# Optimization experiments

Measured on AMD Instinct MI355X. Metric: run time of the kernel, lower is better.

Reference implementation:

```python
import jax, jax.numpy as jnp
import numpy as np

B, S, H = 4, 2048, 1024
NH = 16
HD = H // NH  # 64
EPS = 1e-12


def setup_inputs() -> dict:
    key = jax.random.key(0)
    ks = jax.random.split(key, 10)
    sc = 1.0 / np.sqrt(H)
    return {
        "hidden_states": jax.random.normal(ks[0], (B, S, H), jnp.float32),
        "attention_mask": jnp.ones((B, S), jnp.float32),
        "Wq": jax.random.normal(ks[1], (H, H), jnp.float32) * sc,
        "bq": jnp.zeros((H,), jnp.float32),
        "Wk": jax.random.normal(ks[2], (H, H), jnp.float32) * sc,
        "bk": jnp.zeros((H,), jnp.float32),
        "Wv": jax.random.normal(ks[3], (H, H), jnp.float32) * sc,
        "bv": jnp.zeros((H,), jnp.float32),
        "Wd": jax.random.normal(ks[4], (H, H), jnp.float32) * sc,
        "bd": jnp.zeros((H,), jnp.float32),
        "ln_g": jnp.ones((H,), jnp.float32),
        "ln_b": jnp.zeros((H,), jnp.float32),
    }


def reference(hidden_states, attention_mask, Wq, bq, Wk, bk, Wv, bv, Wd, bd, ln_g, ln_b):
    def heads(x):  # [B,S,H] -> [B,NH,S,HD]
        return x.reshape(B, S, NH, HD).transpose(0, 2, 1, 3)

    q = heads(hidden_states @ Wq.T + bq)
    k = heads(hidden_states @ Wk.T + bk)
    v = heads(hidden_states @ Wv.T + bv)

    scores = jnp.einsum('bhqd,bhkd->bhqk', q, k) / np.sqrt(HD).astype(np.float32)
    # 2D mask -> [B,1,1,S]; (1-m)*-10000 additive bias
    bias = (1.0 - attention_mask)[:, None, None, :] * -10000.0
    probs = jax.nn.softmax(scores + bias, axis=-1)  # dropout p=0 -> identity

    ctx = jnp.einsum('bhqk,bhkd->bhqd', probs, v)
    ctx = ctx.transpose(0, 2, 1, 3).reshape(B, S, H)

    out = ctx @ Wd.T + bd
    x = out + hidden_states
    mu = jnp.mean(x, axis=-1, keepdims=True)
    var = jnp.mean(jnp.square(x - mu), axis=-1, keepdims=True)
    return (x - mu) * jax.lax.rsqrt(var + EPS) * ln_g + ln_b
```

## Files before the change

### kernel.cpp

```cpp
#include <hip/hip_runtime.h>
#include <stdint.h>

#define B_ 4
#define S_ 2048
#define H_ 1024
#define NH_ 16
#define HD_ 64

typedef __bf16 bf16x8 __attribute__((ext_vector_type(8)));
typedef unsigned short u16x8 __attribute__((ext_vector_type(8)));
typedef float f32x4 __attribute__((ext_vector_type(4)));
typedef float f32x16 __attribute__((ext_vector_type(16)));

__device__ __forceinline__ unsigned short f2bf(float x) {
  union { float f; unsigned u; } c; c.f = x;
  unsigned r = (c.u + 0x7FFFu + ((c.u >> 16) & 1u)) >> 16;
  return (unsigned short)r;
}

__device__ __forceinline__ void gload16(const unsigned short* g, unsigned short* lds) {
  __builtin_amdgcn_global_load_lds((const __attribute__((address_space(1))) void*)g,
                                   (__attribute__((address_space(3))) void*)lds, 16, 0, 0);
}

__global__ __launch_bounds__(256) void cvt_kernel(const float* __restrict__ src,
                                                  unsigned short* __restrict__ dst, int n) {
  int i = (blockIdx.x * blockDim.x + threadIdx.x) * 4;
  if (i < n) {
    float4 v = *reinterpret_cast<const float4*>(src + i);
    ushort4 o;
    o.x = f2bf(v.x); o.y = f2bf(v.y); o.z = f2bf(v.z); o.w = f2bf(v.w);
    *reinterpret_cast<ushort4*>(dst + i) = o;
  }
}

template <bool BF16OUT>
__global__ __launch_bounds__(256) void gemm_bt(const unsigned short* __restrict__ A,
                                               const unsigned short* __restrict__ Bm,
                                               const float* __restrict__ bias,
                                               void* __restrict__ Cout,
                                               int M, int N, int K) {
  __shared__ unsigned short As[128 * 32];
  __shared__ unsigned short Bs[128 * 32];
  const int t = threadIdx.x;
  const int lane = t & 63;
  const int wv = t >> 6;
  const int wm = wv >> 1, wn = wv & 1;
  const int m0 = blockIdx.x * 128, n0 = blockIdx.y * 128;
  const int l15 = lane & 15, g8 = (lane >> 4) * 8;

  f32x4 acc[4][4];
#pragma unroll
  for (int i = 0; i < 4; ++i)
#pragma unroll
    for (int j = 0; j < 4; ++j) { f32x4 z = {0.f, 0.f, 0.f, 0.f}; acc[i][j] = z; }

  const int rowA = t >> 2;
  const int colA = (t & 3) * 8;
  const unsigned short* gA0 = A + (long)(m0 + rowA) * K + colA;
  const unsigned short* gA1 = A + (long)(m0 + 64 + rowA) * K + colA;
  const unsigned short* gB0 = Bm + (long)(n0 + rowA) * K + colA;
  const unsigned short* gB1 = Bm + (long)(n0 + 64 + rowA) * K + colA;
  unsigned short* ldsA0 = &As[wv * 512];
  unsigned short* ldsA1 = &As[2048 + wv * 512];
  unsigned short* ldsB0 = &Bs[wv * 512];
  unsigned short* ldsB1 = &Bs[2048 + wv * 512];

  for (int k0 = 0; k0 < K; k0 += 32) {
    __syncthreads();
    gload16(gA0 + k0, ldsA0);
    gload16(gA1 + k0, ldsA1);
    gload16(gB0 + k0, ldsB0);
    gload16(gB1 + k0, ldsB1);
    __syncthreads();

    bf16x8 af[4], bfr[4];
#pragma unroll
    for (int i = 0; i < 4; ++i)
      af[i] = *reinterpret_cast<const bf16x8*>(&As[(wm * 64 + i * 16 + l15) * 32 + g8]);
#pragma unroll
    for (int j = 0; j < 4; ++j)
      bfr[j] = *reinterpret_cast<const bf16x8*>(&Bs[(wn * 64 + j * 16 + l15) * 32 + g8]);
#pragma unroll
    for (int i = 0; i < 4; ++i)
#pragma unroll
      for (int j = 0; j < 4; ++j)
        acc[i][j] = __builtin_amdgcn_mfma_f32_16x16x32_bf16(af[i], bfr[j], acc[i][j], 0, 0, 0);
  }

  const int r0 = (lane >> 4) * 4;
#pragma unroll
  for (int i = 0; i < 4; ++i)
#pragma unroll
    for (int j = 0; j < 4; ++j) {
      int col = n0 + wn * 64 + j * 16 + l15;
      float bv = bias[col];
#pragma unroll
      for (int r = 0; r < 4; ++r) {
        int row = m0 + wm * 64 + i * 16 + r0 + r;
        float v = acc[i][j][r] + bv;
        if (BF16OUT)
          ((unsigned short*)Cout)[(long)row * N + col] = f2bf(v);
        else
          ((float*)Cout)[(long)row * N + col] = v;
      }
    }
}

__global__ __launch_bounds__(256) void attn_kernel(const unsigned short* __restrict__ Q,
                                                   const unsigned short* __restrict__ Kg,
                                                   const unsigned short* __restrict__ Vg,
                                                   const float* __restrict__ mask,
                                                   unsigned short* __restrict__ ctx) {
  __shared__ __align__(16) unsigned short Kt[2][64 * 72];
  __shared__ __align__(16) unsigned short VtT[2][64 * 72];
  __shared__ __align__(16) float biasL[2][64];
  __shared__ __align__(16) float alBuf[4][32];
  __shared__ int mflag[2];

  const int t = threadIdx.x, lane = t & 63;
  const int wv = t >> 6;
  const int h = blockIdx.y, b = blockIdx.z;
  const int q0w = blockIdx.x * 128 + wv * 32;
  const int l31 = lane & 31, h2 = lane >> 5;
  const long headoff = (long)h * HD_;
  const float L2E = 1.44269504088896f;
  const float SC = 0.125f * L2E;

  bf16x8 qf[4];
  {
    const unsigned short* Qrow = Q + ((long)(b * S_ + q0w + l31)) * H_ + headoff;
#pragma unroll
    for (int c = 0; c < 4; ++c) {
      bf16x8 raw = *reinterpret_cast<const bf16x8*>(Qrow + 16 * c + 8 * h2);
#pragma unroll
      for (int j = 0; j < 8; ++j) qf[c][j] = (__bf16)((float)raw[j] * SC);
    }
  }

  f32x16 o[2];
#pragma unroll
  for (int dt = 0; dt < 2; ++dt)
#pragma unroll
    for (int r = 0; r < 16; ++r) o[dt][r] = 0.f;
  float mrow = -1.0e30f, lsum = 0.f;

  const int rowd0 = l31, rowd1 = 32 + l31;
  const int grp0 = (rowd0 >> 3) & 7, grp1 = (rowd1 >> 3) & 7;

  const int krow = t >> 3, kcg = (t & 7) * 8;
  const int vrow = (t >> 3) * 2, dc = t & 7;
  const long gbase = (long)(b * S_) * H_ + headoff;
  u16x8 kr0, kr1, vr0, vr1;
  float mv = 1.0f;

  auto LOADT = [&](int kv0) {
    kr0 = *reinterpret_cast<const u16x8*>(Kg + gbase + (long)(kv0 + krow) * H_ + kcg);
    kr1 = *reinterpret_cast<const u16x8*>(Kg + gbase + (long)(kv0 + krow + 32) * H_ + kcg);
    vr0 = *reinterpret_cast<const u16x8*>(Vg + gbase + (long)(kv0 + vrow) * H_ + dc * 8);
    vr1 = *reinterpret_cast<const u16x8*>(Vg + gbase + (long)(kv0 + vrow + 1) * H_ + dc * 8);
    if (t < 64) mv = mask[b * S_ + kv0 + t];
  };
  auto WRITET = [&](int buf) {
    *reinterpret_cast<u16x8*>(&Kt[buf][krow * 72 + kcg]) = kr0;
    *reinterpret_cast<u16x8*>(&Kt[buf][(krow + 32) * 72 + kcg]) = kr1;
    const int pos = (vrow & 7) | (((vrow >> 3) ^ dc) << 3);
#pragma unroll
    for (int j = 0; j < 8; ++j) {
      ushort2 pr; pr.x = vr0[j]; pr.y = vr1[j];
      *reinterpret_cast<ushort2*>(&VtT[buf][(dc * 8 + j) * 72 + pos]) = pr;
    }
    if (t < 64) {
      biasL[buf][t] = (1.f - mv) * (-10000.f * L2E);
      unsigned long long bal = __ballot(mv != 1.0f);
      if (t == 0) mflag[buf] = (bal != 0ull);
    }
  };

  const int NT = S_ / 64;
  LOADT(0);
  WRITET(0);
  __syncthreads();

  for (int it = 0; it < NT; ++it) {
    const int cur = it & 1;
    const bool more = (it + 1 < NT);
    if (more) LOADT((it + 1) * 64);

    const unsigned short* KtA = &Kt[cur][l31 * 72 + 8 * h2];
    const int mf = mflag[cur];

#pragma unroll
    for (int kvt = 0; kvt < 2; ++kvt) {
      f32x16 sv;
#pragma unroll
      for (int r = 0; r < 16; ++r) sv[r] = 0.f;
      __builtin_amdgcn_s_setprio(1);
#pragma unroll
      for (int c = 0; c < 4; ++c) {
        bf16x8 af = *reinterpret_cast<const bf16x8*>(KtA + (kvt * 32) * 72 + 16 * c);
        sv = __builtin_amdgcn_mfma_f32_32x32x16_bf16(af, qf[c], sv, 0, 0, 0);
      }
      __builtin_amdgcn_s_setprio(0);
      if (mf) {
#pragma unroll
        for (int m = 0; m < 4; ++m) {
          f32x4 bb = *reinterpret_cast<const f32x4*>(&biasL[cur][kvt * 32 + 8 * m + 4 * h2]);
#pragma unroll
          for (int i = 0; i < 4; ++i) sv[4 * m + i] += bb[i];
        }
      }
      float a0 = fmaxf(sv[0], sv[1]), a1 = fmaxf(sv[2], sv[3]);
      float a2 = fmaxf(sv[4], sv[5]), a3 = fmaxf(sv[6], sv[7]);
      float a4 = fmaxf(sv[8], sv[9]), a5 = fmaxf(sv[10], sv[11]);
      float a6 = fmaxf(sv[12], sv[13]), a7 = fmaxf(sv[14], sv[15]);
      float b0 = fmaxf(a0, a1), b1 = fmaxf(a2, a3), b2 = fmaxf(a4, a5), b3 = fmaxf(a6, a7);
      float tm = fmaxf(fmaxf(b0, b1), fmaxf(b2, b3));
      tm = fmaxf(tm, __shfl_xor(tm, 32));
      if (!__all(tm <= mrow + 8.0f)) {
        float mn = fmaxf(mrow, tm);
        float al = exp2f(mrow - mn);
        mrow = mn;
        lsum *= al;
        if (lane < 32) alBuf[wv][lane] = al;
        __builtin_amdgcn_wave_barrier();
#pragma unroll
        for (int m = 0; m < 4; ++m) {
          f32x4 av = *reinterpret_cast<const f32x4*>(&alBuf[wv][8 * m + 4 * h2]);
#pragma unroll
          for (int i = 0; i < 4; ++i) {
            o[0][4 * m + i] *= av[i];
            o[1][4 * m + i] *= av[i];
          }
        }
      }
#pragma unroll
      for (int r = 0; r < 16; ++r) sv[r] = exp2f(sv[r] - mrow);
      {
        float s0 = sv[0] + sv[1], s1 = sv[2] + sv[3], s2 = sv[4] + sv[5], s3 = sv[6] + sv[7];
        float s4 = sv[8] + sv[9], s5 = sv[10] + sv[11], s6 = sv[12] + sv[13], s7 = sv[14] + sv[15];
        float u0 = s0 + s1, u1 = s2 + s3, u2 = s4 + s5, u3 = s6 + s7;
        float ts = (u0 + u1) + (u2 + u3);
        ts += __shfl_xor(ts, 32);
        lsum += ts;
      }

#pragma unroll
      for (int c2 = 0; c2 < 2; ++c2) {
        int kc = 2 * kvt + c2;
        unsigned p0, p1, p2, p3;
        {
          union { __bf16 e[2]; unsigned w; } u;
          u.e[0] = (__bf16)sv[8 * c2 + 0]; u.e[1] = (__bf16)sv[8 * c2 + 1]; p0 = u.w;
          u.e[0] = (__bf16)sv[8 * c2 + 2]; u.e[1] = (__bf16)sv[8 * c2 + 3]; p1 = u.w;
          u.e[0] = (__bf16)sv[8 * c2 + 4]; u.e[1] = (__bf16)sv[8 * c2 + 5]; p2 = u.w;
          u.e[0] = (__bf16)sv[8 * c2 + 6]; u.e[1] = (__bf16)sv[8 * c2 + 7]; p3 = u.w;
        }
        asm("v_permlane32_swap_b32 %0, %1" : "+v"(p0), "+v"(p2));
        asm("v_permlane32_swap_b32 %0, %1" : "+v"(p1), "+v"(p3));
        union { unsigned w[4]; bf16x8 v; } fa;
        fa.w[0] = p0; fa.w[1] = p1; fa.w[2] = p2; fa.w[3] = p3;

        bf16x8 vb0 = *reinterpret_cast<const bf16x8*>(
            &VtT[cur][rowd0 * 72 + 8 * ((2 * kc + h2) ^ grp0)]);
        bf16x8 vb1 = *reinterpret_cast<const bf16x8*>(
            &VtT[cur][rowd1 * 72 + 8 * ((2 * kc + h2) ^ grp1)]);
        __builtin_amdgcn_s_setprio(1);
        o[0] = __builtin_amdgcn_mfma_f32_32x32x16_bf16(fa.v, vb0, o[0], 0, 0, 0);
        o[1] = __builtin_amdgcn_mfma_f32_32x32x16_bf16(fa.v, vb1, o[1], 0, 0, 0);
        __builtin_amdgcn_s_setprio(0);
      }
    }

    if (more) {
      WRITET(cur ^ 1);
      __syncthreads();
    }
  }

  if (lane < 32) alBuf[wv][lane] = 1.0f / lsum;
  __builtin_amdgcn_wave_barrier();
  unsigned short* ctxbase = ctx + ((long)(b * S_ + q0w + 4 * h2)) * H_ + headoff + l31;
#pragma unroll
  for (int m = 0; m < 4; ++m) {
    f32x4 iv = *reinterpret_cast<const f32x4*>(&alBuf[wv][8 * m + 4 * h2]);
#pragma unroll
    for (int i = 0; i < 4; ++i) {
#pragma unroll
      for (int dt = 0; dt < 2; ++dt)
        ctxbase[(long)(8 * m + i) * H_ + dt * 32] = f2bf(o[dt][4 * m + i] * iv[i]);
    }
  }
}

__global__ __launch_bounds__(256) void ln_kernel(const float* __restrict__ proj,
                                                 const float* __restrict__ hs,
                                                 const float* __restrict__ gam,
                                                 const float* __restrict__ bet,
                                                 float* __restrict__ out) {
  const int row = blockIdx.x;
  const int t = threadIdx.x;
  const long base = (long)row * H_ + t * 4;
  float4 a = *reinterpret_cast<const float4*>(proj + base);
  float4 hv = *reinterpret_cast<const float4*>(hs + base);
  float x0 = a.x + hv.x, x1 = a.y + hv.y, x2 = a.z + hv.z, x3 = a.w + hv.w;
  float s1 = x0 + x1 + x2 + x3;
  float s2 = x0 * x0 + x1 * x1 + x2 * x2 + x3 * x3;
#pragma unroll
  for (int off = 1; off < 64; off <<= 1) {
    s1 += __shfl_xor(s1, off);
    s2 += __shfl_xor(s2, off);
  }
  __shared__ float a1[4], a2[4];
  if ((t & 63) == 0) { a1[t >> 6] = s1; a2[t >> 6] = s2; }
  __syncthreads();
  float ts1 = a1[0] + a1[1] + a1[2] + a1[3];
  float ts2 = a2[0] + a2[1] + a2[2] + a2[3];
  float mu = ts1 * (1.0f / H_);
  float var = ts2 * (1.0f / H_) - mu * mu;
  float inv = rsqrtf(var + 1e-12f);
  float4 gv = *reinterpret_cast<const float4*>(gam + t * 4);
  float4 bb = *reinterpret_cast<const float4*>(bet + t * 4);
  float4 ov;
  ov.x = (x0 - mu) * inv * gv.x + bb.x;
  ov.y = (x1 - mu) * inv * gv.y + bb.y;
  ov.z = (x2 - mu) * inv * gv.z + bb.z;
  ov.w = (x3 - mu) * inv * gv.w + bb.w;
  *reinterpret_cast<float4*>(out + base) = ov;
}

extern "C" void kernel_launch(void* const* d_in, const int* in_sizes, int n_in,
                              void* d_out, int out_size, void* d_ws, size_t ws_size,
                              hipStream_t stream) {
  const float* hs   = (const float*)d_in[0];
  const float* mask = (const float*)d_in[1];
  const float* Wq   = (const float*)d_in[2];
  const float* bq   = (const float*)d_in[3];
  const float* Wk   = (const float*)d_in[4];
  const float* bk   = (const float*)d_in[5];
  const float* Wv   = (const float*)d_in[6];
  const float* bv   = (const float*)d_in[7];
  const float* Wd   = (const float*)d_in[8];
  const float* bd   = (const float*)d_in[9];
  const float* lng  = (const float*)d_in[10];
  const float* lnb  = (const float*)d_in[11];
  float* out = (float*)d_out;

  char* ws = (char*)d_ws;
  const size_t SZ_X = (size_t)B_ * S_ * H_ * 2;
  const size_t SZ_W = (size_t)H_ * H_ * 2;
  unsigned short* Xb  = (unsigned short*)(ws);
  unsigned short* Wqb = (unsigned short*)(ws + SZ_X);
  unsigned short* Wkb = (unsigned short*)(ws + SZ_X + SZ_W);
  unsigned short* Wvb = (unsigned short*)(ws + SZ_X + 2 * SZ_W);
  unsigned short* Wdb = (unsigned short*)(ws + SZ_X + 3 * SZ_W);
  unsigned short* Qb  = (unsigned short*)(ws + SZ_X + 4 * SZ_W);
  unsigned short* Kb  = (unsigned short*)(ws + 2 * SZ_X + 4 * SZ_W);
  unsigned short* Vb  = (unsigned short*)(ws + 3 * SZ_X + 4 * SZ_W);
  unsigned short* Cxb = (unsigned short*)(ws + 4 * SZ_X + 4 * SZ_W);
  float* Proj         = (float*)(ws + 5 * SZ_X + 4 * SZ_W);

  const int NX = B_ * S_ * H_;
  const int NW = H_ * H_;

  cvt_kernel<<<NX / 1024, 256, 0, stream>>>(hs, Xb, NX);
  cvt_kernel<<<NW / 1024, 256, 0, stream>>>(Wq, Wqb, NW);
  cvt_kernel<<<NW / 1024, 256, 0, stream>>>(Wk, Wkb, NW);
  cvt_kernel<<<NW / 1024, 256, 0, stream>>>(Wv, Wvb, NW);
  cvt_kernel<<<NW / 1024, 256, 0, stream>>>(Wd, Wdb, NW);

  dim3 gg(B_ * S_ / 128, H_ / 128);
  gemm_bt<true><<<gg, 256, 0, stream>>>(Xb, Wqb, bq, Qb, B_ * S_, H_, H_);
  gemm_bt<true><<<gg, 256, 0, stream>>>(Xb, Wkb, bk, Kb, B_ * S_, H_, H_);
  gemm_bt<true><<<gg, 256, 0, stream>>>(Xb, Wvb, bv, Vb, B_ * S_, H_, H_);

  dim3 ga(S_ / 128, NH_, B_);
  attn_kernel<<<ga, 256, 0, stream>>>(Qb, Kb, Vb, mask, Cxb);

  gemm_bt<false><<<gg, 256, 0, stream>>>(Cxb, Wdb, bd, Proj, B_ * S_, H_, H_);

  ln_kernel<<<B_ * S_, 256, 0, stream>>>(Proj, hs, lng, lnb, out);
}
```

Before: 311.9 us.

## Skip mask loads when unmasked, batch weight casts, restructure attention softmax loop

Each attention block now scans the full mask row once up front. When every entry is one, it skips the per-tile mask loads and bias writes. Both QK^T MFMA groups for a tile are now issued before the softmax/PV stage, which moves into a lambda. The change also adds packed bf16 conversion via v_cvt_pk_bf16_f32, precomputed V LDS offsets and a launch_bounds occupancy hint, and merges the four weight-conversion launches into one grid. The up-front mask scan and extra syncs add overhead per block, and holding two score tiles live at once raises register pressure.

```diff
diff --git a/kernel.cpp b/kernel.cpp
--- a/kernel.cpp
+++ b/kernel.cpp
@@ -18,6 +18,12 @@
   return (unsigned short)r;
 }
 
+__device__ __forceinline__ unsigned cvtpk(float lo, float hi) {
+  unsigned r;
+  asm("v_cvt_pk_bf16_f32 %0, %1, %2" : "=v"(r) : "v"(lo), "v"(hi));
+  return r;
+}
+
 __device__ __forceinline__ void gload16(const unsigned short* g, unsigned short* lds) {
   __builtin_amdgcn_global_load_lds((const __attribute__((address_space(1))) void*)g,
                                    (__attribute__((address_space(3))) void*)lds, 16, 0, 0);
@@ -25,6 +31,26 @@
 
 __global__ __launch_bounds__(256) void cvt_kernel(const float* __restrict__ src,
                                                   unsigned short* __restrict__ dst, int n) {
+  int i = (blockIdx.x * blockDim.x + threadIdx.x) * 4;
+  if (i < n) {
+    float4 v = *reinterpret_cast<const float4*>(src + i);
+    ushort4 o;
+    o.x = f2bf(v.x); o.y = f2bf(v.y); o.z = f2bf(v.z); o.w = f2bf(v.w);
+    *reinterpret_cast<ushort4*>(dst + i) = o;
+  }
+}
+
+__global__ __launch_bounds__(256) void cvtw_kernel(const float* __restrict__ w0,
+                                                   const float* __restrict__ w1,
+                                                   const float* __restrict__ w2,
+                                                   const float* __restrict__ w3,
+                                                   unsigned short* __restrict__ o0,
+                                                   unsigned short* __restrict__ o1,
+                                                   unsigned short* __restrict__ o2,
+                                                   unsigned short* __restrict__ o3, int n) {
+  const int which = blockIdx.y;
+  const float* src = (which == 0) ? w0 : (which == 1) ? w1 : (which == 2) ? w2 : w3;
+  unsigned short* dst = (which == 0) ? o0 : (which == 1) ? o1 : (which == 2) ? o2 : o3;
   int i = (blockIdx.x * blockDim.x + threadIdx.x) * 4;
   if (i < n) {
     float4 v = *reinterpret_cast<const float4*>(src + i);
@@ -107,16 +133,17 @@
     }
 }
 
-__global__ __launch_bounds__(256) void attn_kernel(const unsigned short* __restrict__ Q,
-                                                   const unsigned short* __restrict__ Kg,
-                                                   const unsigned short* __restrict__ Vg,
-                                                   const float* __restrict__ mask,
-                                                   unsigned short* __restrict__ ctx) {
+__global__ __launch_bounds__(256, 4) void attn_kernel(const unsigned short* __restrict__ Q,
+                                                      const unsigned short* __restrict__ Kg,
+                                                      const unsigned short* __restrict__ Vg,
+                                                      const float* __restrict__ mask,
+                                                      unsigned short* __restrict__ ctx) {
   __shared__ __align__(16) unsigned short Kt[2][64 * 72];
   __shared__ __align__(16) unsigned short VtT[2][64 * 72];
   __shared__ __align__(16) float biasL[2][64];
   __shared__ __align__(16) float alBuf[4][32];
   __shared__ int mflag[2];
+  __shared__ int anyMsh;
 
   const int t = threadIdx.x, lane = t & 63;
   const int wv = t >> 6;
@@ -127,6 +154,14 @@
   const float L2E = 1.44269504088896f;
   const float SC = 0.125f * L2E;
 
+  if (t == 0) anyMsh = 0;
+  __syncthreads();
+  {
+    bool nz = false;
+    for (int i = t; i < S_; i += 256) nz |= (mask[(long)b * S_ + i] != 1.0f);
+    if (__any(nz) && lane == 0) atomicOr(&anyMsh, 1);
+  }
+
   bf16x8 qf[4];
   {
     const unsigned short* Qrow = Q + ((long)(b * S_ + q0w + l31)) * H_ + headoff;
@@ -137,6 +172,8 @@
       for (int j = 0; j < 8; ++j) qf[c][j] = (__bf16)((float)raw[j] * SC);
     }
   }
+  __syncthreads();
+  const bool anyM = (anyMsh != 0);
 
   f32x16 o[2];
 #pragma unroll
@@ -147,21 +184,26 @@
 
   const int rowd0 = l31, rowd1 = 32 + l31;
   const int grp0 = (rowd0 >> 3) & 7, grp1 = (rowd1 >> 3) & 7;
+
+  int voff0[4], voff1[4];
+#pragma unroll
+  for (int kc = 0; kc < 4; ++kc) {
+    voff0[kc] = rowd0 * 72 + 8 * ((2 * kc + h2) ^ grp0);
+    voff1[kc] = rowd1 * 72 + 8 * ((2 * kc + h2) ^ grp1);
+  }
 
   const int krow = t >> 3, kcg = (t & 7) * 8;
   const int vrow = (t >> 3) * 2, dc = t & 7;
   const long gbase = (long)(b * S_) * H_ + headoff;
   u16x8 kr0, kr1, vr0, vr1;
-  float mv = 1.0f;
 
   auto LOADT = [&](int kv0) {
     kr0 = *reinterpret_cast<const u16x8*>(Kg + gbase + (long)(kv0 + krow) * H_ + kcg);
     kr1 = *reinterpret_cast<const u16x8*>(Kg + gbase + (long)(kv0 + krow + 32) * H_ + kcg);
     vr0 = *reinterpret_cast<const u16x8*>(Vg + gbase + (long)(kv0 + vrow) * H_ + dc * 8);
     vr1 = *reinterpret_cast<const u16x8*>(Vg + gbase + (long)(kv0 + vrow + 1) * H_ + dc * 8);
-    if (t < 64) mv = mask[b * S_ + kv0 + t];
   };
-  auto WRITET = [&](int buf) {
+  auto WRITET = [&](int buf, int kv0) {
     *reinterpret_cast<u16x8*>(&Kt[buf][krow * 72 + kcg]) = kr0;
     *reinterpret_cast<u16x8*>(&Kt[buf][(krow + 32) * 72 + kcg]) = kr1;
     const int pos = (vrow & 7) | (((vrow >> 3) ^ dc) << 3);
@@ -170,16 +212,75 @@
       ushort2 pr; pr.x = vr0[j]; pr.y = vr1[j];
       *reinterpret_cast<ushort2*>(&VtT[buf][(dc * 8 + j) * 72 + pos]) = pr;
     }
-    if (t < 64) {
+    if (anyM && t < 64) {
+      float mv = mask[(long)b * S_ + kv0 + t];
       biasL[buf][t] = (1.f - mv) * (-10000.f * L2E);
       unsigned long long bal = __ballot(mv != 1.0f);
       if (t == 0) mflag[buf] = (bal != 0ull);
     }
   };
 
+  auto SMPV = [&](f32x16& sv, int kvt, int cur) {
+    float m0 = fmaxf(fmaxf(sv[0], sv[1]), sv[2]);
+    float m1 = fmaxf(fmaxf(sv[3], sv[4]), sv[5]);
+    float m2 = fmaxf(fmaxf(sv[6], sv[7]), sv[8]);
+    float m3 = fmaxf(fmaxf(sv[9], sv[10]), sv[11]);
+    float m4 = fmaxf(fmaxf(sv[12], sv[13]), sv[14]);
+    float t0 = fmaxf(fmaxf(m0, m1), m2);
+    float t1 = fmaxf(fmaxf(m3, m4), sv[15]);
+    float tm = fmaxf(t0, t1);
+    tm = fmaxf(tm, __shfl_xor(tm, 32));
+    if (!__all(tm <= mrow + 8.0f)) {
+      float mn = fmaxf(mrow, tm);
+      float al = exp2f(mrow - mn);
+      mrow = mn;
+      lsum *= al;
+      if (lane < 32) alBuf[wv][lane] = al;
+      __builtin_amdgcn_wave_barrier();
+#pragma unroll
+      for (int m = 0; m < 4; ++m) {
+        f32x4 av = *reinterpret_cast<const f32x4*>(&alBuf[wv][8 * m + 4 * h2]);
+#pragma unroll
+        for (int i = 0; i < 4; ++i) {
+          o[0][4 * m + i] *= av[i];
+          o[1][4 * m + i] *= av[i];
+        }
+      }
+    }
+#pragma unroll
+    for (int r = 0; r < 16; ++r) sv[r] = exp2f(sv[r] - mrow);
+    {
+      float s0 = sv[0] + sv[1], s1 = sv[2] + sv[3], s2 = sv[4] + sv[5], s3 = sv[6] + sv[7];
+      float s4 = sv[8] + sv[9], s5 = sv[10] + sv[11], s6 = sv[12] + sv[13], s7 = sv[14] + sv[15];
+      float u0 = s0 + s1, u1 = s2 + s3, u2 = s4 + s5, u3 = s6 + s7;
+      float ts = (u0 + u1) + (u2 + u3);
+      ts += __shfl_xor(ts, 32);
+      lsum += ts;
+    }
+#pragma unroll
+    for (int c2 = 0; c2 < 2; ++c2) {
+      const int kc = 2 * kvt + c2;
+      unsigned p0 = cvtpk(sv[8 * c2 + 0], sv[8 * c2 + 1]);
+      unsigned p1 = cvtpk(sv[8 * c2 + 2], sv[8 * c2 + 3]);
+      unsigned p2 = cvtpk(sv[8 * c2 + 4], sv[8 * c2 + 5]);
+      unsigned p3 = cvtpk(sv[8 * c2 + 6], sv[8 * c2 + 7]);
+      asm("v_permlane32_swap_b32 %0, %1" : "+v"(p0), "+v"(p2));
+      asm("v_permlane32_swap_b32 %0, %1" : "+v"(p1), "+v"(p3));
+      union { unsigned w[4]; bf16x8 v; } fa;
+      fa.w[0] = p0; fa.w[1] = p1; fa.w[2] = p2; fa.w[3] = p3;
+
+      bf16x8 vb0 = *reinterpret_cast<const bf16x8*>(&VtT[cur][voff0[kc]]);
+      bf16x8 vb1 = *reinterpret_cast<const bf16x8*>(&VtT[cur][voff1[kc]]);
+      __builtin_amdgcn_s_setprio(1);
+      o[0] = __builtin_amdgcn_mfma_f32_32x32x16_bf16(fa.v, vb0, o[0], 0, 0, 0);
+      o[1] = __builtin_amdgcn_mfma_f32_32x32x16_bf16(fa.v, vb1, o[1], 0, 0, 0);
+      __builtin_amdgcn_s_setprio(0);
+    }
+  };
+
   const int NT = S_ / 64;
   LOADT(0);
-  WRITET(0);
+  WRITET(0, 0);
   __syncthreads();
 
   for (int it = 0; it < NT; ++it) {
@@ -188,92 +289,38 @@
     if (more) LOADT((it + 1) * 64);
 
     const unsigned short* KtA = &Kt[cur][l31 * 72 + 8 * h2];
-    const int mf = mflag[cur];
-
-#pragma unroll
-    for (int kvt = 0; kvt < 2; ++kvt) {
-      f32x16 sv;
-#pragma unroll
-      for (int r = 0; r < 16; ++r) sv[r] = 0.f;
-      __builtin_amdgcn_s_setprio(1);
-#pragma unroll
-      for (int c = 0; c < 4; ++c) {
-        bf16x8 af = *reinterpret_cast<const bf16x8*>(KtA + (kvt * 32) * 72 + 16 * c);
-        sv = __builtin_amdgcn_mfma_f32_32x32x16_bf16(af, qf[c], sv, 0, 0, 0);
+
+    f32x16 sv0, sv1;
+#pragma unroll
+    for (int r = 0; r < 16; ++r) { sv0[r] = 0.f; sv1[r] = 0.f; }
+    __builtin_amdgcn_s_setprio(1);
+#pragma unroll
+    for (int c = 0; c < 4; ++c) {
+      bf16x8 af = *reinterpret_cast<const bf16x8*>(KtA + 16 * c);
+      sv0 = __builtin_amdgcn_mfma_f32_32x32x16_bf16(af, qf[c], sv0, 0, 0, 0);
+    }
+#pragma unroll
+    for (int c = 0; c < 4; ++c) {
+      bf16x8 af = *reinterpret_cast<const bf16x8*>(KtA + 32 * 72 + 16 * c);
+      sv1 = __builtin_amdgcn_mfma_f32_32x32x16_bf16(af, qf[c], sv1, 0, 0, 0);
+    }
+    __builtin_amdgcn_s_setprio(0);
+
+    if (anyM && mflag[cur]) {
+#pragma unroll
+      for (int m = 0; m < 4; ++m) {
+        f32x4 b0 = *reinterpret_cast<const f32x4*>(&biasL[cur][8 * m + 4 * h2]);
+        f32x4 b1 = *reinterpret_cast<const f32x4*>(&biasL[cur][32 + 8 * m + 4 * h2]);
+#pragma unroll
+        for (int i = 0; i < 4; ++i) { sv0[4 * m + i] += b0[i]; sv1[4 * m + i] += b1[i]; }
       }
-      __builtin_amdgcn_s_setprio(0);
-      if (mf) {
-#pragma unroll
-        for (int m = 0; m < 4; ++m) {
-          f32x4 bb = *reinterpret_cast<const f32x4*>(&biasL[cur][kvt * 32 + 8 * m + 4 * h2]);
-#pragma unroll
-          for (int i = 0; i < 4; ++i) sv[4 * m + i] += bb[i];
-        }
-      }
-      float a0 = fmaxf(sv[0], sv[1]), a1 = fmaxf(sv[2], sv[3]);
-      float a2 = fmaxf(sv[4], sv[5]), a3 = fmaxf(sv[6], sv[7]);
-      float a4 = fmaxf(sv[8], sv[9]), a5 = fmaxf(sv[10], sv[11]);
-      float a6 = fmaxf(sv[12], sv[13]), a7 = fmaxf(sv[14], sv[15]);
-      float b0 = fmaxf(a0, a1), b1 = fmaxf(a2, a3), b2 = fmaxf(a4, a5), b3 = fmaxf(a6, a7);
-      float tm = fmaxf(fmaxf(b0, b1), fmaxf(b2, b3));
-      tm = fmaxf(tm, __shfl_xor(tm, 32));
-      if (!__all(tm <= mrow + 8.0f)) {
-        float mn = fmaxf(mrow, tm);
-        float al = exp2f(mrow - mn);
-        mrow = mn;
-        lsum *= al;
-        if (lane < 32) alBuf[wv][lane] = al;
-        __builtin_amdgcn_wave_barrier();
-#pragma unroll
-        for (int m = 0; m < 4; ++m) {
-          f32x4 av = *reinterpret_cast<const f32x4*>(&alBuf[wv][8 * m + 4 * h2]);
-#pragma unroll
-          for (int i = 0; i < 4; ++i) {
-            o[0][4 * m + i] *= av[i];
-            o[1][4 * m + i] *= av[i];
-          }
-        }
-      }
-#pragma unroll
-      for (int r = 0; r < 16; ++r) sv[r] = exp2f(sv[r] - mrow);
-      {
-        float s0 = sv[0] + sv[1], s1 = sv[2] + sv[3], s2 = sv[4] + sv[5], s3 = sv[6] + sv[7];
-        float s4 = sv[8] + sv[9], s5 = sv[10] + sv[11], s6 = sv[12] + sv[13], s7 = sv[14] + sv[15];
-        float u0 = s0 + s1, u1 = s2 + s3, u2 = s4 + s5, u3 = s6 + s7;
-        float ts = (u0 + u1) + (u2 + u3);
-        ts += __shfl_xor(ts, 32);
-        lsum += ts;
-      }
-
-#pragma unroll
-      for (int c2 = 0; c2 < 2; ++c2) {
-        int kc = 2 * kvt + c2;
-        unsigned p0, p1, p2, p3;
-        {
-          union { __bf16 e[2]; unsigned w; } u;
-          u.e[0] = (__bf16)sv[8 * c2 + 0]; u.e[1] = (__bf16)sv[8 * c2 + 1]; p0 = u.w;
-          u.e[0] = (__bf16)sv[8 * c2 + 2]; u.e[1] = (__bf16)sv[8 * c2 + 3]; p1 = u.w;
-          u.e[0] = (__bf16)sv[8 * c2 + 4]; u.e[1] = (__bf16)sv[8 * c2 + 5]; p2 = u.w;
-          u.e[0] = (__bf16)sv[8 * c2 + 6]; u.e[1] = (__bf16)sv[8 * c2 + 7]; p3 = u.w;
-        }
-        asm("v_permlane32_swap_b32 %0, %1" : "+v"(p0), "+v"(p2));
-        asm("v_permlane32_swap_b32 %0, %1" : "+v"(p1), "+v"(p3));
-        union { unsigned w[4]; bf16x8 v; } fa;
-        fa.w[0] = p0; fa.w[1] = p1; fa.w[2] = p2; fa.w[3] = p3;
-
-        bf16x8 vb0 = *reinterpret_cast<const bf16x8*>(
-            &VtT[cur][rowd0 * 72 + 8 * ((2 * kc + h2) ^ grp0)]);
-        bf16x8 vb1 = *reinterpret_cast<const bf16x8*>(
-            &VtT[cur][rowd1 * 72 + 8 * ((2 * kc + h2) ^ grp1)]);
-        __builtin_amdgcn_s_setprio(1);
-        o[0] = __builtin_amdgcn_mfma_f32_32x32x16_bf16(fa.v, vb0, o[0], 0, 0, 0);
-        o[1] = __builtin_amdgcn_mfma_f32_32x32x16_bf16(fa.v, vb1, o[1], 0, 0, 0);
-        __builtin_amdgcn_s_setprio(0);
-      }
-    }
+    }
+
+    SMPV(sv0, 0, cur);
+    SMPV(sv1, 1, cur);
 
     if (more) {
-      WRITET(cur ^ 1);
+      WRITET(cur ^ 1, (it + 1) * 64);
       __syncthreads();
     }
   }
@@ -364,10 +411,8 @@
   const int NW = H_ * H_;
 
   cvt_kernel<<<NX / 1024, 256, 0, stream>>>(hs, Xb, NX);
-  cvt_kernel<<<NW / 1024, 256, 0, stream>>>(Wq, Wqb, NW);
-  cvt_kernel<<<NW / 1024, 256, 0, stream>>>(Wk, Wkb, NW);
-  cvt_kernel<<<NW / 1024, 256, 0, stream>>>(Wv, Wvb, NW);
-  cvt_kernel<<<NW / 1024, 256, 0, stream>>>(Wd, Wdb, NW);
+  dim3 gw(NW / 1024, 4);
+  cvtw_kernel<<<gw, 256, 0, stream>>>(Wq, Wk, Wv, Wd, Wqb, Wkb, Wvb, Wdb, NW);
 
   dim3 gg(B_ * S_ / 128, H_ / 128);
   gemm_bt<true><<<gg, 256, 0, stream>>>(Xb, Wqb, bq, Qb, B_ * S_, H_, H_);
```

After: 320.1 us. 2.6% more time.
